# Optimization experiments

Measured on AMD Instinct MI355X. Metric: run time of the kernel, lower is better.

## Reference

```python
import jax, jax.numpy as jnp
import numpy as np

B, N, C, H = 4, 2048, 256, 16
D = C // H  # head dim = 16


def setup_inputs() -> dict:
    key = jax.random.key(0)
    k1, k2, k3 = jax.random.split(key, 3)
    x = jax.random.normal(k1, (B, N, C), dtype=jnp.float32)
    w_qkv = jax.random.normal(k2, (C, 3 * C), dtype=jnp.float32) * (C ** -0.5)
    b_qkv = jnp.zeros((3 * C,), dtype=jnp.float32)
    w_proj = jax.random.normal(k3, (C, C), dtype=jnp.float32) * (C ** -0.5)
    b_proj = jnp.zeros((C,), dtype=jnp.float32)
    return {"x": x, "w_qkv": w_qkv, "b_qkv": b_qkv, "w_proj": w_proj, "b_proj": b_proj}


def reference(x, w_qkv, b_qkv, w_proj, b_proj):
    b, n, c = x.shape
    qkv = x @ w_qkv + b_qkv                       # (B, N, 3C)
    qkv = qkv.reshape(b, n, 3, H, D)
    q = jnp.transpose(qkv[:, :, 0], (0, 2, 1, 3))  # (B, H, N, D)
    k = jnp.transpose(qkv[:, :, 1], (0, 2, 1, 3))
    v = jnp.transpose(qkv[:, :, 2], (0, 2, 1, 3))
    # NOTE: the original module applies NO 1/sqrt(d) scaling.
    attn = jnp.einsum('bhqd,bhkd->bhqk', q, k)     # (B, H, N, N)
    attn = jax.nn.softmax(attn, axis=-1)
    out = jnp.einsum('bhqk,bhkd->bhqd', attn, v)   # (B, H, N, D)
    out = jnp.transpose(out, (0, 2, 1, 3)).reshape(b, n, c)
    return out @ w_proj + b_proj
```

## Files before the change

### kernel.cpp

```cpp
#include <hip/hip_runtime.h>
#include <stdint.h>

typedef __attribute__((ext_vector_type(8))) short short8;
typedef __attribute__((ext_vector_type(4))) short short4v;
typedef __attribute__((ext_vector_type(4))) float float4v;
typedef __attribute__((ext_vector_type(16))) float float16v;
typedef __attribute__((ext_vector_type(4))) uint32_t uint4v;

__device__ __forceinline__ short f2bf(float f) {
    union { float f; uint32_t u; } v; v.f = f;
    uint32_t u = v.u;
    uint32_t r = (u + 0x7fffu + ((u >> 16) & 1u)) >> 16;
    return (short)r;
}

#if __has_builtin(__builtin_amdgcn_cvt_pk_bf16_f32)
typedef __bf16 bf16x2_t __attribute__((ext_vector_type(2)));
__device__ __forceinline__ uint32_t cvt_pk2(float a, float b) {
    union { bf16x2_t v; uint32_t u; } c;
    c.v = __builtin_amdgcn_cvt_pk_bf16_f32(a, b);
    return c.u;
}
#else
__device__ __forceinline__ uint32_t cvt_pk2(float a, float b) {
    union { float f; uint32_t u; } x, y; x.f = a; y.f = b;
    return ((x.u + 0x8000u) >> 16) | ((y.u + 0x8000u) & 0xFFFF0000u);
}
#endif


__global__ __launch_bounds__(256) void cvt_bf16_kernel(const float* __restrict__ in,
                                                       short* __restrict__ out, int n) {
    int i = (blockIdx.x * 256 + threadIdx.x) * 4;
    if (i < n) {
        float4 v = *(const float4*)(in + i);
        short4v o;
        o.x = f2bf(v.x); o.y = f2bf(v.y); o.z = f2bf(v.z); o.w = f2bf(v.w);
        *(short4v*)(out + i) = o;
    }
}

__global__ __launch_bounds__(256) void cvtT_kernel(const float* __restrict__ in,
                                                   short* __restrict__ out, int N, int total) {
    int idx = blockIdx.x * 256 + threadIdx.x;
    if (idx < total) {
        int n = idx >> 8, k = idx & 255;
        out[idx] = f2bf(in[k * N + n]);
    }
}


template<int MODE>
__global__ __launch_bounds__(256) void gemm_kernel(
    const short* __restrict__ A, const short* __restrict__ Bt,
    const float* __restrict__ bias,
    short* __restrict__ outQ, short* __restrict__ outK, short* __restrict__ outV,
    float* __restrict__ outP)
{
    const int K = 256;
    int m0 = blockIdx.x * 64;
    int n0 = blockIdx.y * 64;
    int tid = threadIdx.x;
    int wave = tid >> 6, lane = tid & 63, quad = lane >> 4, lc = lane & 15;

    __shared__ __align__(16) short As[64 * 48];
    __shared__ __align__(16) short Bs[64 * 48];

    float4v acc[4];
    #pragma unroll
    for (int t = 0; t < 4; ++t) acc[t] = (float4v){0.f, 0.f, 0.f, 0.f};

    int srow = tid >> 2, sseg = tid & 3;

    for (int c = 0; c < K; c += 32) {
        __syncthreads();
        *(short8*)(&As[srow * 48 + sseg * 8]) =
            *(const short8*)(A + (size_t)(m0 + srow) * K + c + sseg * 8);
        *(short8*)(&Bs[srow * 48 + sseg * 8]) =
            *(const short8*)(Bt + (size_t)(n0 + srow) * K + c + sseg * 8);
        __syncthreads();

        short8 af = *(short8*)(&As[(wave * 16 + lc) * 48 + quad * 8]);
        #pragma unroll
        for (int t = 0; t < 4; ++t) {
            short8 bf = *(short8*)(&Bs[(t * 16 + lc) * 48 + quad * 8]);
            acc[t] = __builtin_amdgcn_mfma_f32_16x16x32_bf16(af, bf, acc[t], 0, 0, 0);
        }
    }

    #pragma unroll
    for (int t = 0; t < 4; ++t) {
        int cg = n0 + t * 16 + lc;
        float bv = bias[cg];
        #pragma unroll
        for (int r = 0; r < 4; ++r) {
            int rg = m0 + wave * 16 + quad * 4 + r;
            float val = acc[t][r] + bv;
            if (MODE == 0) {
                int s = cg >> 8, rem = cg & 255, h = rem >> 4, d = rem & 15;
                int b = rg >> 11, n = rg & 2047;
                if (s == 0) val *= 1.4426950408889634f;
                short* dst = (s == 0) ? outQ : ((s == 1) ? outK : outV);
                dst[((((size_t)b * 16 + h) * 2048 + n) << 4) + d] = f2bf(val);
            } else {
                outP[(size_t)rg * 256 + cg] = val;
            }
        }
    }
}


__global__ __launch_bounds__(256) void attn_kernel(
    const short* __restrict__ Q, const short* __restrict__ Kp, const short* __restrict__ V,
    short* __restrict__ Out)
{
    const int N = 2048;
    int bh = blockIdx.y;
    int b = bh >> 4, h = bh & 15;
    int tid = threadIdx.x;
    int wave = tid >> 6, lane = tid & 63;
    int m = lane & 31, hi = lane >> 5;
    int qbase = blockIdx.x * 128 + wave * 32;

    const short* Qh = Q + (size_t)bh * N * 16;
    const short* Kh = Kp + (size_t)bh * N * 16;
    const short* Vh = V + (size_t)bh * N * 16;

    __shared__ __align__(16) short Vt[16][264];

    short8 qf = *(const short8*)(Qh + (size_t)(qbase + m) * 16 + hi * 8);

    short8 ones, zeros;
    #pragma unroll
    for (int j = 0; j < 8; ++j) { ones[j] = (short)0x3F80; zeros[j] = 0; }

    float16v Oacc, zf;
    #pragma unroll
    for (int j = 0; j < 16; ++j) { Oacc[j] = 0.f; zf[j] = 0.f; }

    int sd = tid & 15, sa = tid >> 4;
    int kb = ((sa & 1) << 3) | (((sa >> 1) & 1) << 2) | ((sa >> 2) << 4);

    for (int sc = 0; sc < N; sc += 256) {
        __syncthreads();
        #pragma unroll
        for (int cc = 0; cc < 4; ++cc) {
            const short* vp = Vh + (size_t)(sc + cc * 64 + kb) * 16 + sd;
            short4v pack;
            pack.x = vp[0]; pack.y = vp[16]; pack.z = vp[32]; pack.w = vp[48];
            *(short4v*)(&Vt[sd][cc * 64 + sa * 4]) = pack;
        }
        __syncthreads();

        #pragma unroll
        for (int it = 0; it < 4; ++it) {
            int c = sc + it * 64;
            short8 kf1 = *(const short8*)(Kh + (size_t)(c + m) * 16 + hi * 8);
            short8 kf2 = *(const short8*)(Kh + (size_t)(c + 32 + m) * 16 + hi * 8);

            float16v S1 = __builtin_amdgcn_mfma_f32_32x32x16_bf16(kf1, qf, zf, 0, 0, 0);
            float16v S2 = __builtin_amdgcn_mfma_f32_32x32x16_bf16(kf2, qf, zf, 0, 0, 0);

            union { uint4v u; short8 s; } pA, pB, pC, pD;
            pA.u = (uint4v){
                cvt_pk2(__builtin_amdgcn_exp2f(S1[0]), __builtin_amdgcn_exp2f(S1[1])),
                cvt_pk2(__builtin_amdgcn_exp2f(S1[2]), __builtin_amdgcn_exp2f(S1[3])),
                cvt_pk2(__builtin_amdgcn_exp2f(S1[4]), __builtin_amdgcn_exp2f(S1[5])),
                cvt_pk2(__builtin_amdgcn_exp2f(S1[6]), __builtin_amdgcn_exp2f(S1[7]))};
            pB.u = (uint4v){
                cvt_pk2(__builtin_amdgcn_exp2f(S1[8]),  __builtin_amdgcn_exp2f(S1[9])),
                cvt_pk2(__builtin_amdgcn_exp2f(S1[10]), __builtin_amdgcn_exp2f(S1[11])),
                cvt_pk2(__builtin_amdgcn_exp2f(S1[12]), __builtin_amdgcn_exp2f(S1[13])),
                cvt_pk2(__builtin_amdgcn_exp2f(S1[14]), __builtin_amdgcn_exp2f(S1[15]))};
            pC.u = (uint4v){
                cvt_pk2(__builtin_amdgcn_exp2f(S2[0]), __builtin_amdgcn_exp2f(S2[1])),
                cvt_pk2(__builtin_amdgcn_exp2f(S2[2]), __builtin_amdgcn_exp2f(S2[3])),
                cvt_pk2(__builtin_amdgcn_exp2f(S2[4]), __builtin_amdgcn_exp2f(S2[5])),
                cvt_pk2(__builtin_amdgcn_exp2f(S2[6]), __builtin_amdgcn_exp2f(S2[7]))};
            pD.u = (uint4v){
                cvt_pk2(__builtin_amdgcn_exp2f(S2[8]),  __builtin_amdgcn_exp2f(S2[9])),
                cvt_pk2(__builtin_amdgcn_exp2f(S2[10]), __builtin_amdgcn_exp2f(S2[11])),
                cvt_pk2(__builtin_amdgcn_exp2f(S2[12]), __builtin_amdgcn_exp2f(S2[13])),
                cvt_pk2(__builtin_amdgcn_exp2f(S2[14]), __builtin_amdgcn_exp2f(S2[15]))};

            #pragma unroll
            for (int p = 0; p < 4; ++p) {
                short8 vf;
                if (m < 16)      vf = *(const short8*)(&Vt[m][it * 64 + p * 16 + hi * 8]);
                else if (m == 16) vf = ones;
                else              vf = zeros;
                short8 pf = (p == 0) ? pA.s : (p == 1) ? pB.s : (p == 2) ? pC.s : pD.s;
                Oacc = __builtin_amdgcn_mfma_f32_32x32x16_bf16(vf, pf, Oacc, 0, 0, 0);
            }
        }
    }

    float Lq = __shfl(Oacc[8], m, 64);
    float inv = 1.0f / Lq;
    uint32_t o0 = cvt_pk2(Oacc[0] * inv, Oacc[1] * inv);
    uint32_t o1 = cvt_pk2(Oacc[2] * inv, Oacc[3] * inv);
    uint32_t o2 = cvt_pk2(Oacc[4] * inv, Oacc[5] * inv);
    uint32_t o3 = cvt_pk2(Oacc[6] * inv, Oacc[7] * inv);
    short* row = Out + ((size_t)(b * 2048 + qbase + m)) * 256 + h * 16;
    uint2 w0; w0.x = o0; w0.y = o1;
    uint2 w1; w1.x = o2; w1.y = o3;
    *(uint2*)(row + hi * 4) = w0;
    *(uint2*)(row + 8 + hi * 4) = w1;
}


extern "C" void kernel_launch(void* const* d_in, const int* in_sizes, int n_in,
                              void* d_out, int out_size, void* d_ws, size_t ws_size,
                              hipStream_t stream) {
    const float* x      = (const float*)d_in[0];
    const float* w_qkv  = (const float*)d_in[1];
    const float* b_qkv  = (const float*)d_in[2];
    const float* w_proj = (const float*)d_in[3];
    const float* b_proj = (const float*)d_in[4];
    float* out = (float*)d_out;

    short* xb     = (short*)d_ws;
    short* wqkvT  = xb + 2097152;
    short* wprojT = wqkvT + 196608;
    short* Qb     = wprojT + 65536;
    short* Kb     = Qb + 2097152;
    short* Vb     = Kb + 2097152;
    short* Ab     = Vb + 2097152;

    cvt_bf16_kernel<<<2048, 256, 0, stream>>>(x, xb, 2097152);
    cvtT_kernel<<<768, 256, 0, stream>>>(w_qkv, wqkvT, 768, 196608);
    cvtT_kernel<<<256, 256, 0, stream>>>(w_proj, wprojT, 256, 65536);

    gemm_kernel<0><<<dim3(128, 12), 256, 0, stream>>>(xb, wqkvT, b_qkv, Qb, Kb, Vb, nullptr);

    attn_kernel<<<dim3(16, 64), 256, 0, stream>>>(Qb, Kb, Vb, Ab);

    gemm_kernel<1><<<dim3(128, 4), 256, 0, stream>>>(Ab, wprojT, b_proj,
                                                     nullptr, nullptr, nullptr, out);
}
```

Measured before the change: 141.2 us.

## Fuse x bf16 conversion into QKV GEMM, merge weight converts, LDS ones-row

Drops the separate x-to-bf16 pass: the QKV GEMM now reads fp32 x directly and converts to bf16 while staging into LDS. The two weight-transpose conversions become one launch, so there are two fewer kernel launches and no bf16 copy of x written and re-read. In the attention kernel the ones/zeros rows used to accumulate the softmax denominator now live in an extended LDS tile, which removes the per-lane branch before each MFMA. In exchange the GEMM reads twice the bytes for A (12 column blocks each re-read fp32 x), and attention uses more shared memory.

```diff
diff --git a/kernel.cpp b/kernel.cpp
--- a/kernel.cpp
+++ b/kernel.cpp
@@ -29,30 +29,25 @@
 #endif
 
 
-__global__ __launch_bounds__(256) void cvt_bf16_kernel(const float* __restrict__ in,
-                                                       short* __restrict__ out, int n) {
-    int i = (blockIdx.x * 256 + threadIdx.x) * 4;
-    if (i < n) {
-        float4 v = *(const float4*)(in + i);
-        short4v o;
-        o.x = f2bf(v.x); o.y = f2bf(v.y); o.z = f2bf(v.z); o.w = f2bf(v.w);
-        *(short4v*)(out + i) = o;
-    }
-}
-
-__global__ __launch_bounds__(256) void cvtT_kernel(const float* __restrict__ in,
-                                                   short* __restrict__ out, int N, int total) {
+__global__ __launch_bounds__(256) void cvtW_kernel(const float* __restrict__ wqkv,
+                                                   const float* __restrict__ wproj,
+                                                   short* __restrict__ outq,
+                                                   short* __restrict__ outp) {
     int idx = blockIdx.x * 256 + threadIdx.x;
-    if (idx < total) {
+    if (idx < 196608) {
         int n = idx >> 8, k = idx & 255;
-        out[idx] = f2bf(in[k * N + n]);
+        outq[idx] = f2bf(wqkv[k * 768 + n]);
+    } else {
+        int i = idx - 196608;
+        int n = i >> 8, k = i & 255;
+        outp[i] = f2bf(wproj[k * 256 + n]);
     }
 }
 
 
 template<int MODE>
 __global__ __launch_bounds__(256) void gemm_kernel(
-    const short* __restrict__ A, const short* __restrict__ Bt,
+    const void* __restrict__ Ap, const short* __restrict__ Bt,
     const float* __restrict__ bias,
     short* __restrict__ outQ, short* __restrict__ outK, short* __restrict__ outV,
     float* __restrict__ outP)
@@ -74,8 +69,17 @@
 
     for (int c = 0; c < K; c += 32) {
         __syncthreads();
-        *(short8*)(&As[srow * 48 + sseg * 8]) =
-            *(const short8*)(A + (size_t)(m0 + srow) * K + c + sseg * 8);
+        if (MODE == 0) {
+            const float* src = (const float*)Ap + (size_t)(m0 + srow) * K + c + sseg * 8;
+            float4 f0 = *(const float4*)src;
+            float4 f1 = *(const float4*)(src + 4);
+            uint4v u; u.x = cvt_pk2(f0.x, f0.y); u.y = cvt_pk2(f0.z, f0.w);
+            u.z = cvt_pk2(f1.x, f1.y); u.w = cvt_pk2(f1.z, f1.w);
+            *(uint4v*)(&As[srow * 48 + sseg * 8]) = u;
+        } else {
+            *(short8*)(&As[srow * 48 + sseg * 8]) =
+                *(const short8*)((const short*)Ap + (size_t)(m0 + srow) * K + c + sseg * 8);
+        }
         *(short8*)(&Bs[srow * 48 + sseg * 8]) =
             *(const short8*)(Bt + (size_t)(n0 + srow) * K + c + sseg * 8);
         __syncthreads();
@@ -126,13 +130,20 @@
     const short* Kh = Kp + (size_t)bh * N * 16;
     const short* Vh = V + (size_t)bh * N * 16;
 
-    __shared__ __align__(16) short Vt[16][264];
+    __shared__ __align__(16) short Vt[32][264];
+
+    {
+        int r = 16 + (tid >> 4);
+        int c0 = (tid & 15) * 16;
+        short fill = (r == 16) ? (short)0x3F80 : (short)0;
+        short8 f8;
+        #pragma unroll
+        for (int j = 0; j < 8; ++j) f8[j] = fill;
+        *(short8*)(&Vt[r][c0]) = f8;
+        *(short8*)(&Vt[r][c0 + 8]) = f8;
+    }
 
     short8 qf = *(const short8*)(Qh + (size_t)(qbase + m) * 16 + hi * 8);
-
-    short8 ones, zeros;
-    #pragma unroll
-    for (int j = 0; j < 8; ++j) { ones[j] = (short)0x3F80; zeros[j] = 0; }
 
     float16v Oacc, zf;
     #pragma unroll
@@ -185,10 +196,7 @@
 
             #pragma unroll
             for (int p = 0; p < 4; ++p) {
-                short8 vf;
-                if (m < 16)      vf = *(const short8*)(&Vt[m][it * 64 + p * 16 + hi * 8]);
-                else if (m == 16) vf = ones;
-                else              vf = zeros;
+                short8 vf = *(const short8*)(&Vt[m][it * 64 + p * 16 + hi * 8]);
                 short8 pf = (p == 0) ? pA.s : (p == 1) ? pB.s : (p == 2) ? pC.s : pD.s;
                 Oacc = __builtin_amdgcn_mfma_f32_32x32x16_bf16(vf, pf, Oacc, 0, 0, 0);
             }
@@ -219,19 +227,16 @@
     const float* b_proj = (const float*)d_in[4];
     float* out = (float*)d_out;
 
-    short* xb     = (short*)d_ws;
-    short* wqkvT  = xb + 2097152;
+    short* wqkvT  = (short*)d_ws;
     short* wprojT = wqkvT + 196608;
     short* Qb     = wprojT + 65536;
     short* Kb     = Qb + 2097152;
     short* Vb     = Kb + 2097152;
     short* Ab     = Vb + 2097152;
 
-    cvt_bf16_kernel<<<2048, 256, 0, stream>>>(x, xb, 2097152);
-    cvtT_kernel<<<768, 256, 0, stream>>>(w_qkv, wqkvT, 768, 196608);
-    cvtT_kernel<<<256, 256, 0, stream>>>(w_proj, wprojT, 256, 65536);
-
-    gemm_kernel<0><<<dim3(128, 12), 256, 0, stream>>>(xb, wqkvT, b_qkv, Qb, Kb, Vb, nullptr);
+    cvtW_kernel<<<1024, 256, 0, stream>>>(w_qkv, w_proj, wqkvT, wprojT);
+
+    gemm_kernel<0><<<dim3(128, 12), 256, 0, stream>>>(x, wqkvT, b_qkv, Qb, Kb, Vb, nullptr);
 
     attn_kernel<<<dim3(16, 64), 256, 0, stream>>>(Qb, Kb, Vb, Ab);
 
```

New measurement: 139.9 us. No clear change (-1.0%).
